# Kernel tuning notes

Hardware: AMD Instinct MI355X
Metric: run time of the kernel (lower is better)

## Reference

```python
import jax, jax.numpy as jnp
import numpy as np

D, H, E, C, B = 1024, 2048, 8, 1024, 8192


def setup_inputs() -> dict:
    key = jax.random.key(0)
    ks = jax.random.split(key, 12)
    s_d = 1.0 / np.sqrt(D)
    s_h = 1.0 / np.sqrt(H)
    return {
        "x": jax.random.normal(ks[0], (B, D), dtype=jnp.float32),
        # gate (Router): Linear(D,D) -> relu -> Linear(D,E) -> softmax
        "gate_w1": jax.random.normal(ks[1], (D, D), dtype=jnp.float32) * s_d,
        "gate_b1": jax.random.normal(ks[2], (D,), dtype=jnp.float32) * s_d,
        "gate_w2": jax.random.normal(ks[3], (D, E), dtype=jnp.float32) * s_d,
        "gate_b2": jax.random.normal(ks[4], (E,), dtype=jnp.float32) * s_d,
        # experts stacked: fc1 [E,D,H], fc2 [E,H,H]
        "W1": jax.random.normal(ks[5], (E, D, H), dtype=jnp.float32) * s_d,
        "b1": jax.random.normal(ks[6], (E, H), dtype=jnp.float32) * s_d,
        "W2": jax.random.normal(ks[7], (E, H, H), dtype=jnp.float32) * s_h,
        "b2": jax.random.normal(ks[8], (E, H), dtype=jnp.float32) * s_h,
        # classifier Linear(H, C)
        "clf_w": jax.random.normal(ks[9], (H, C), dtype=jnp.float32) * s_h,
        "clf_b": jax.random.normal(ks[10], (C,), dtype=jnp.float32) * s_h,
    }


def reference(x, gate_w1, gate_b1, gate_w2, gate_b2, W1, b1, W2, b2, clf_w, clf_b):
    # Router: softmax over experts (dim=1)
    g = jax.nn.relu(x @ gate_w1 + gate_b1)          # [B, D]
    scores = jax.nn.softmax(g @ gate_w2 + gate_b2, axis=1)  # [B, E]

    # All experts, dense (training-mode forward): batched GEMMs over E
    h = jax.nn.relu(jnp.einsum('bd,edh->beh', x, W1) + b1[None])   # [B, E, H]
    expert_outs = jnp.einsum('beh,ehk->bek', h, W2) + b2[None]      # [B, E, H]

    # Shared classifier applied per (token, expert)
    logits = jnp.einsum('beh,hc->bec', expert_outs, clf_w) + clf_b  # [B, E, C]
    return logits, scores
```

## Files before the change

kernel.cpp:

```cpp
#include <hip/hip_runtime.h>
#include <stdint.h>

#define B_DIM 8192
#define D_DIM 1024
#define H_DIM 2048
#define E_DIM 8
#define C_DIM 1024

typedef _Float16 f16x8 __attribute__((ext_vector_type(8)));
typedef float f32x4 __attribute__((ext_vector_type(4)));

__device__ __forceinline__ void store_val(float* p, float v) { *p = v; }
__device__ __forceinline__ void store_val(_Float16* p, float v) { *p = (_Float16)v; }

__device__ __forceinline__ void async_cp16(const void* g, void* l) {
  __builtin_amdgcn_global_load_lds((const __attribute__((address_space(1))) void*)g,
                                   (__attribute__((address_space(3))) void*)l, 16, 0, 0);
}

template <bool RELU, bool BIAS, typename OUT_T>
__global__ void __launch_bounds__(256) gemm_bt(
    const _Float16* __restrict__ A, long aZ,
    const _Float16* __restrict__ Bt, long bZ,
    const float* __restrict__ bias, long biasZ,
    OUT_T* __restrict__ out, long outZ,
    int K, long rs)
{
  __shared__ _Float16 ldsA[128 * 64];
  __shared__ _Float16 ldsB[128 * 64];

  const int z = blockIdx.z;
  A   += (size_t)z * aZ;
  Bt  += (size_t)z * bZ;
  if (BIAS) bias += (size_t)z * biasZ;
  out += (size_t)z * outZ;

  const int tid  = threadIdx.x;
  const int wave = tid >> 6;
  const int lane = tid & 63;
  const int q    = lane >> 4;
  const int l16  = lane & 15;
  const int l8   = lane >> 3;
  const int l7   = lane & 7;

  const int m0   = blockIdx.y * 128;
  const int n0   = blockIdx.x * 128;
  const int wrow = (wave >> 1) * 64;
  const int wcol = (wave & 1) * 64;

  const int swz_st = ((l7 ^ l8) << 3);
  const _Float16* pa[4];
  const _Float16* pb[4];
#pragma unroll
  for (int i = 0; i < 4; ++i) {
    int ci = wave * 4 + i;
    pa[i] = A  + (size_t)(m0 + ci * 8 + l8) * K + swz_st;
    pb[i] = Bt + (size_t)(n0 + ci * 8 + l8) * K + swz_st;
  }

  int a_off[2][4], b_off[2][4];
#pragma unroll
  for (int kk = 0; kk < 2; ++kk) {
#pragma unroll
    for (int r = 0; r < 4; ++r) {
      int sw = ((kk * 4 + q) ^ (l16 & 7)) << 4;
      a_off[kk][r] = (wrow + r * 16 + l16) * 128 + sw;
      b_off[kk][r] = (wcol + r * 16 + l16) * 128 + sw;
    }
  }

  f32x4 acc[4][4];
#pragma unroll
  for (int r = 0; r < 4; ++r)
#pragma unroll
    for (int c = 0; c < 4; ++c)
      acc[r][c] = (f32x4){0.f, 0.f, 0.f, 0.f};

  const char* lAc = (const char*)ldsA;
  const char* lBc = (const char*)ldsB;

  for (int kt = 0; kt < K; kt += 64) {
    __syncthreads();
#pragma unroll
    for (int i = 0; i < 4; ++i) {
      int ci = wave * 4 + i;
      async_cp16(pa[i], ldsA + ci * 512);
      async_cp16(pb[i], ldsB + ci * 512);
      pa[i] += 64;
      pb[i] += 64;
    }
    __syncthreads();
#pragma unroll
    for (int kk = 0; kk < 2; ++kk) {
      f16x8 af[4], bfv[4];
#pragma unroll
      for (int r = 0; r < 4; ++r) af[r]  = *(const f16x8*)(lAc + a_off[kk][r]);
#pragma unroll
      for (int c = 0; c < 4; ++c) bfv[c] = *(const f16x8*)(lBc + b_off[kk][c]);
#pragma unroll
      for (int r = 0; r < 4; ++r)
#pragma unroll
        for (int c = 0; c < 4; ++c)
          acc[r][c] = __builtin_amdgcn_mfma_f32_16x16x32_f16(af[r], bfv[c], acc[r][c], 0, 0, 0);
    }
  }

#pragma unroll
  for (int c = 0; c < 4; ++c) {
    int col = n0 + wcol + c * 16 + l16;
    float bv = BIAS ? bias[col] : 0.f;
#pragma unroll
    for (int r = 0; r < 4; ++r) {
      int row = m0 + wrow + r * 16 + q * 4;
      f32x4 v = acc[r][c];
#pragma unroll
      for (int i = 0; i < 4; ++i) {
        float xv = v[i] + bv;
        if (RELU) xv = fmaxf(xv, 0.f);
        store_val(out + (size_t)(row + i) * rs + col, xv);
      }
    }
  }
}

template <bool RELU, bool BIAS, typename OUT_T>
__global__ void __launch_bounds__(512) gemm256(
    const _Float16* __restrict__ A, long aZ,
    const _Float16* __restrict__ Bt, long bZ,
    const float* __restrict__ bias, long biasZ,
    OUT_T* __restrict__ out, long outZ,
    int K, long rs)
{
  __shared__ _Float16 ldsA[2 * 256 * 64];
  __shared__ _Float16 ldsB[2 * 256 * 64];

  const int z = blockIdx.z;
  A   += (size_t)z * aZ;
  Bt  += (size_t)z * bZ;
  if (BIAS) bias += (size_t)z * biasZ;
  out += (size_t)z * outZ;

  const int nwg = gridDim.x * gridDim.y;
  const int wg  = blockIdx.y * gridDim.x + blockIdx.x;
  const int sw  = (wg & 7) * (nwg >> 3) + (wg >> 3);
  const int bx  = sw % gridDim.x;
  const int by  = sw / gridDim.x;

  const int tid  = threadIdx.x;
  const int wave = tid >> 6;
  const int lane = tid & 63;
  const int q    = lane >> 4;
  const int l16  = lane & 15;
  const int l8   = lane >> 3;
  const int l7   = lane & 7;

  const int m0   = by * 256;
  const int n0   = bx * 256;
  const int wm   = wave >> 2;
  const int wn   = wave & 3;
  const int wrow = wm * 128;
  const int wcol = wn * 64;

  const int swz_st = ((l7 ^ l8) << 3);
  const _Float16* paB = A  + (size_t)(m0 + wave * 16 + l8) * K + swz_st;
  const _Float16* pbB = Bt + (size_t)(n0 + wave * 16 + l8) * K + swz_st;

  int a_base[2], b_base[2];
#pragma unroll
  for (int kk = 0; kk < 2; ++kk) {
    int swr = (((kk * 4 + q) ^ (l16 & 7)) << 4);
    a_base[kk] = (wrow + l16) * 128 + swr;
    b_base[kk] = (wcol + l16) * 128 + swr;
  }

  f32x4 acc[8][4];
#pragma unroll
  for (int r = 0; r < 8; ++r)
#pragma unroll
    for (int c = 0; c < 4; ++c)
      acc[r][c] = (f32x4){0.f, 0.f, 0.f, 0.f};

  const char* lA = (const char*)ldsA;
  const char* lB = (const char*)ldsB;
  const int NT = K >> 6;

#define STAGE_A(buf, h, tt)                                                          \
  {                                                                                  \
    _Pragma("unroll")                                                                \
    for (int i_ = 0; i_ < 2; ++i_)                                                   \
      async_cp16(paB + (size_t)((h) * 128 + i_ * 8) * K + (tt) * 64,                 \
                 (void*)(ldsA + (buf) * 16384 + (h) * 8192 + (wave * 2 + i_) * 512)); \
  }
#define STAGE_B(buf, h, tt)                                                          \
  {                                                                                  \
    _Pragma("unroll")                                                                \
    for (int i_ = 0; i_ < 2; ++i_)                                                   \
      async_cp16(pbB + (size_t)((h) * 128 + i_ * 8) * K + (tt) * 64,                 \
                 (void*)(ldsB + (buf) * 16384 + (h) * 8192 + (wave * 2 + i_) * 512)); \
  }

  STAGE_A(0, 0, 0) STAGE_A(0, 1, 0) STAGE_B(0, 0, 0) STAGE_B(0, 1, 0)
  STAGE_B(1, 0, 1) STAGE_B(1, 1, 1)
  asm volatile("s_waitcnt vmcnt(4)" ::: "memory");
  __builtin_amdgcn_s_barrier();

  for (int t = 0; t < NT; ++t) {
    const int bofs = (t & 1) * 32768;
    f16x8 bf[4][2];
#pragma unroll
    for (int p = 0; p < 4; ++p) {
      f16x8 af[2][2];
#pragma unroll
      for (int rr = 0; rr < 2; ++rr)
#pragma unroll
        for (int kk = 0; kk < 2; ++kk)
          af[rr][kk] = *(const f16x8*)(lA + bofs + a_base[kk] + (2 * p + rr) * 2048);
      if (p == 0) {
#pragma unroll
        for (int c = 0; c < 4; ++c)
#pragma unroll
          for (int kk = 0; kk < 2; ++kk)
            bf[c][kk] = *(const f16x8*)(lB + bofs + b_base[kk] + c * 2048);
      }
      if (p == 0 && t + 1 < NT) STAGE_A((t + 1) & 1, 0, t + 1)
      if (p == 1 && t + 1 < NT) STAGE_A((t + 1) & 1, 1, t + 1)
      if (p == 2 && t + 2 < NT) STAGE_B(t & 1, 0, t + 2)
      if (p == 3 && t + 2 < NT) STAGE_B(t & 1, 1, t + 2)

      __builtin_amdgcn_s_barrier();
      asm volatile("s_waitcnt lgkmcnt(0)" ::: "memory");
      __builtin_amdgcn_sched_barrier(0);
      __builtin_amdgcn_s_setprio(1);
#pragma unroll
      for (int c = 0; c < 4; ++c)
#pragma unroll
        for (int rr = 0; rr < 2; ++rr)
#pragma unroll
          for (int kk = 0; kk < 2; ++kk)
            acc[2 * p + rr][c] = __builtin_amdgcn_mfma_f32_16x16x32_f16(
                af[rr][kk], bf[c][kk], acc[2 * p + rr][c], 0, 0, 0);
      __builtin_amdgcn_s_setprio(0);
      if (p == 3) {
        if (t < NT - 2) asm volatile("s_waitcnt vmcnt(4)" ::: "memory");
        else            asm volatile("s_waitcnt vmcnt(0)" ::: "memory");
      }
      __builtin_amdgcn_s_barrier();
    }
  }
#undef STAGE_A
#undef STAGE_B

#pragma unroll
  for (int c = 0; c < 4; ++c) {
    int col = n0 + wcol + c * 16 + l16;
    float bv = BIAS ? bias[col] : 0.f;
#pragma unroll
    for (int r = 0; r < 8; ++r) {
      int row = m0 + wrow + r * 16 + q * 4;
      f32x4 v = acc[r][c];
#pragma unroll
      for (int i = 0; i < 4; ++i) {
        float xv = v[i] + bv;
        if (RELU) xv = fmaxf(xv, 0.f);
        store_val(out + (size_t)(row + i) * rs + col, xv);
      }
    }
  }
}

__global__ void cast_f32_f16(const float* __restrict__ in, _Float16* __restrict__ out, int n) {
  int i = (blockIdx.x * blockDim.x + threadIdx.x) * 4;
  if (i >= n) return;
  float4 v = *(const float4*)(in + i);
  union { _Float16 h[4]; uint2 u; } r;
  r.h[0] = (_Float16)v.x; r.h[1] = (_Float16)v.y;
  r.h[2] = (_Float16)v.z; r.h[3] = (_Float16)v.w;
  *(uint2*)(out + i) = r.u;
}

__global__ void transpose_cast(const float* __restrict__ in, _Float16* __restrict__ out,
                               int R, int Cn) {
  __shared__ float tile[32][33];
  in  += (size_t)blockIdx.z * R * Cn;
  out += (size_t)blockIdx.z * R * Cn;
  int c0 = blockIdx.x * 32, r0 = blockIdx.y * 32;
  int tx = threadIdx.x, ty = threadIdx.y;
#pragma unroll
  for (int i = ty; i < 32; i += 8)
    tile[i][tx] = in[(size_t)(r0 + i) * Cn + c0 + tx];
  __syncthreads();
#pragma unroll
  for (int i = ty; i < 32; i += 8)
    out[(size_t)(c0 + i) * R + r0 + tx] = (_Float16)tile[tx][i];
}

__global__ void gate2_softmax(const _Float16* __restrict__ g, const float* __restrict__ w2,
                              const float* __restrict__ b2, float* __restrict__ scores) {
  int b = blockIdx.x;
  int t = threadIdx.x;
  int e = t & 7, slice = t >> 3;
  const _Float16* gr = g + (size_t)b * D_DIM;
  float acc = 0.f;
  for (int d = slice; d < D_DIM; d += 32)
    acc += (float)gr[d] * w2[d * 8 + e];
  __shared__ float red[256];
  red[t] = acc;
  __syncthreads();
  for (int s = 16; s > 0; s >>= 1) {
    if (slice < s) red[t] += red[t + s * 8];
    __syncthreads();
  }
  __shared__ float sm[8];
  if (t < 8) sm[t] = red[t] + b2[t];
  __syncthreads();
  if (t == 0) {
    float mx = sm[0];
#pragma unroll
    for (int i = 1; i < 8; ++i) mx = fmaxf(mx, sm[i]);
    float ex[8], s = 0.f;
#pragma unroll
    for (int i = 0; i < 8; ++i) { ex[i] = expf(sm[i] - mx); s += ex[i]; }
    float inv = 1.f / s;
#pragma unroll
    for (int i = 0; i < 8; ++i) scores[(size_t)b * 8 + i] = ex[i] * inv;
  }
}

__global__ void combined_bias(const float* __restrict__ b2, const float* __restrict__ cw,
                              const float* __restrict__ cb, float* __restrict__ bc) {
  int e  = blockIdx.y;
  int cl = threadIdx.x & 63;
  int c  = blockIdx.x * 64 + cl;
  int ks = threadIdx.x >> 6;
  float acc = 0.f;
  for (int k = ks; k < H_DIM; k += 4)
    acc += b2[e * H_DIM + k] * cw[(size_t)k * C_DIM + c];
  __shared__ float red[256];
  red[threadIdx.x] = acc;
  __syncthreads();
  if (ks == 0)
    bc[(size_t)e * C_DIM + c] = red[cl] + red[cl + 64] + red[cl + 128] + red[cl + 192] + cb[c];
}

extern "C" void kernel_launch(void* const* d_in, const int* in_sizes, int n_in,
                              void* d_out, int out_size, void* d_ws, size_t ws_size,
                              hipStream_t stream) {
  const float* x   = (const float*)d_in[0];
  const float* gw1 = (const float*)d_in[1];
  const float* gb1 = (const float*)d_in[2];
  const float* gw2 = (const float*)d_in[3];
  const float* gb2 = (const float*)d_in[4];
  const float* W1  = (const float*)d_in[5];
  const float* b1  = (const float*)d_in[6];
  const float* W2  = (const float*)d_in[7];
  const float* b2  = (const float*)d_in[8];
  const float* cw  = (const float*)d_in[9];
  const float* cb  = (const float*)d_in[10];

  char* ws = (char*)d_ws;
  _Float16* xb     = (_Float16*)(ws);
  _Float16* g      = (_Float16*)(ws + 16777216ull);
  _Float16* gw1t   = (_Float16*)(ws + 33554432ull);
  _Float16* W1t    = (_Float16*)(ws + 35651584ull);
  _Float16* W2c    = (_Float16*)(ws + 69206016ull);
  _Float16* cwt    = (_Float16*)(ws + 136314880ull);
  _Float16* WcombT = (_Float16*)(ws + 140509184ull);
  float*    bc     = (float*)   (ws + 174063616ull);
  _Float16* h_all  = (_Float16*)(ws + 174096384ull);

  float* logits = (float*)d_out;
  float* scores = logits + (size_t)B_DIM * E_DIM * C_DIM;

  cast_f32_f16<<<B_DIM * D_DIM / 4 / 256, 256, 0, stream>>>(x, xb, B_DIM * D_DIM);
  transpose_cast<<<dim3(32, 32, 1), dim3(32, 8), 0, stream>>>(gw1, gw1t, D_DIM, D_DIM);
  transpose_cast<<<dim3(64, 32, 8), dim3(32, 8), 0, stream>>>(W1, W1t, D_DIM, H_DIM);
  cast_f32_f16<<<E_DIM * H_DIM * H_DIM / 4 / 256, 256, 0, stream>>>(W2, W2c, E_DIM * H_DIM * H_DIM);
  transpose_cast<<<dim3(32, 64, 1), dim3(32, 8), 0, stream>>>(cw, cwt, H_DIM, C_DIM);

  gemm_bt<true, true, _Float16><<<dim3(8, 64, 1), 256, 0, stream>>>(
      xb, 0, gw1t, 0, gb1, 0, g, 0, D_DIM, (long)D_DIM);
  gate2_softmax<<<B_DIM, 256, 0, stream>>>(g, gw2, gb2, scores);

  gemm_bt<false, false, _Float16><<<dim3(16, 8, 8), 256, 0, stream>>>(
      cwt, 0, W2c, (long)H_DIM * H_DIM, nullptr, 0,
      WcombT, (long)C_DIM * H_DIM, H_DIM, (long)H_DIM);
  combined_bias<<<dim3(C_DIM / 64, E_DIM), 256, 0, stream>>>(b2, cw, cb, bc);

  gemm256<true, true, _Float16><<<dim3(8, 32, 8), 512, 0, stream>>>(
      xb, 0, W1t, (long)H_DIM * D_DIM, b1, (long)H_DIM,
      h_all, (long)B_DIM * H_DIM, D_DIM, (long)H_DIM);

  gemm256<false, true, float><<<dim3(4, 32, 8), 512, 0, stream>>>(
      h_all, (long)B_DIM * H_DIM, WcombT, (long)C_DIM * H_DIM, bc, (long)C_DIM,
      logits, (long)C_DIM, H_DIM, (long)(E_DIM * C_DIM));
}
```

Baseline: 1.442 ms.

## Template K, restructure gemm256 inner loop, use it for combined-weight GEMM

Makes K a compile-time template parameter and replaces index arithmetic with advancing pointers. The inner loop is reordered to split work by k-half instead of row-pair, keeping fewer fragment registers live. It also drops the mid-phase barrier and waits on LDS reads after the MFMAs rather than before. The classifier-times-W2 combined-weight GEMM moves from the 128-tile gemm_bt to the 256-tile gemm256 kernel. The aim is less register pressure and sync overhead per phase, at the risk of a race on the LDS buffer now that a barrier is gone.

```diff
diff --git a/kernel.cpp b/kernel.cpp
--- a/kernel.cpp
+++ b/kernel.cpp
@@ -123,14 +123,14 @@
   }
 }
 
-template <bool RELU, bool BIAS, typename OUT_T>
+template <bool RELU, bool BIAS, typename OUT_T, int K_CT>
 __global__ void __launch_bounds__(512) gemm256(
     const _Float16* __restrict__ A, long aZ,
     const _Float16* __restrict__ Bt, long bZ,
     const float* __restrict__ bias, long biasZ,
-    OUT_T* __restrict__ out, long outZ,
-    int K, long rs)
+    OUT_T* __restrict__ out, long outZ, long rs)
 {
+  constexpr int NT = K_CT / 64;
   __shared__ _Float16 ldsA[2 * 256 * 64];
   __shared__ _Float16 ldsB[2 * 256 * 64];
 
@@ -162,8 +162,8 @@
   const int wcol = wn * 64;
 
   const int swz_st = ((l7 ^ l8) << 3);
-  const _Float16* paB = A  + (size_t)(m0 + wave * 16 + l8) * K + swz_st;
-  const _Float16* pbB = Bt + (size_t)(n0 + wave * 16 + l8) * K + swz_st;
+  const _Float16* paB = A  + (size_t)(m0 + wave * 16 + l8) * K_CT + swz_st;
+  const _Float16* pbB = Bt + (size_t)(n0 + wave * 16 + l8) * K_CT + swz_st;
 
   int a_base[2], b_base[2];
 #pragma unroll
@@ -182,70 +182,72 @@
 
   const char* lA = (const char*)ldsA;
   const char* lB = (const char*)ldsB;
-  const int NT = K >> 6;
-
-#define STAGE_A(buf, h, tt)                                                          \
-  {                                                                                  \
-    _Pragma("unroll")                                                                \
-    for (int i_ = 0; i_ < 2; ++i_)                                                   \
-      async_cp16(paB + (size_t)((h) * 128 + i_ * 8) * K + (tt) * 64,                 \
-                 (void*)(ldsA + (buf) * 16384 + (h) * 8192 + (wave * 2 + i_) * 512)); \
-  }
-#define STAGE_B(buf, h, tt)                                                          \
-  {                                                                                  \
-    _Pragma("unroll")                                                                \
-    for (int i_ = 0; i_ < 2; ++i_)                                                   \
-      async_cp16(pbB + (size_t)((h) * 128 + i_ * 8) * K + (tt) * 64,                 \
-                 (void*)(ldsB + (buf) * 16384 + (h) * 8192 + (wave * 2 + i_) * 512)); \
-  }
-
-  STAGE_A(0, 0, 0) STAGE_A(0, 1, 0) STAGE_B(0, 0, 0) STAGE_B(0, 1, 0)
-  STAGE_B(1, 0, 1) STAGE_B(1, 1, 1)
+
+#define STAGE_A(bufe, hh, ptr)                                                        \
+  {                                                                                   \
+    _Pragma("unroll")                                                                 \
+    for (int i_ = 0; i_ < 2; ++i_)                                                    \
+      async_cp16((ptr) + (size_t)((hh) * 128 + i_ * 8) * K_CT,                        \
+                 (void*)(ldsA + (bufe) + (hh) * 8192 + (wave * 2 + i_) * 512));       \
+  }
+#define STAGE_B(bufe, hh, ptr)                                                        \
+  {                                                                                   \
+    _Pragma("unroll")                                                                 \
+    for (int i_ = 0; i_ < 2; ++i_)                                                    \
+      async_cp16((ptr) + (size_t)((hh) * 128 + i_ * 8) * K_CT,                        \
+                 (void*)(ldsB + (bufe) + (hh) * 8192 + (wave * 2 + i_) * 512));       \
+  }
+
+  STAGE_A(0, 0, paB) STAGE_A(0, 1, paB)
+  STAGE_B(0, 0, pbB) STAGE_B(0, 1, pbB)
+  STAGE_B(16384, 0, pbB + 64) STAGE_B(16384, 1, pbB + 64)
   asm volatile("s_waitcnt vmcnt(4)" ::: "memory");
   __builtin_amdgcn_s_barrier();
 
+  const _Float16* pa_t = paB + 64;
+  const _Float16* pb_t = pbB + 128;
+
   for (int t = 0; t < NT; ++t) {
-    const int bofs = (t & 1) * 32768;
-    f16x8 bf[4][2];
+    const int bofs  = (t & 1) * 32768;
+    const int nbufe = ((t + 1) & 1) * 16384;
+    const int cbufe = (t & 1) * 16384;
+    f16x8 bf[4];
 #pragma unroll
     for (int p = 0; p < 4; ++p) {
-      f16x8 af[2][2];
-#pragma unroll
-      for (int rr = 0; rr < 2; ++rr)
-#pragma unroll
-        for (int kk = 0; kk < 2; ++kk)
-          af[rr][kk] = *(const f16x8*)(lA + bofs + a_base[kk] + (2 * p + rr) * 2048);
-      if (p == 0) {
+      const int kk = p >> 1, h = p & 1;
+      if (h == 0) {
 #pragma unroll
         for (int c = 0; c < 4; ++c)
-#pragma unroll
-          for (int kk = 0; kk < 2; ++kk)
-            bf[c][kk] = *(const f16x8*)(lB + bofs + b_base[kk] + c * 2048);
+          bf[c] = *(const f16x8*)(lB + bofs + b_base[kk] + c * 2048);
       }
-      if (p == 0 && t + 1 < NT) STAGE_A((t + 1) & 1, 0, t + 1)
-      if (p == 1 && t + 1 < NT) STAGE_A((t + 1) & 1, 1, t + 1)
-      if (p == 2 && t + 2 < NT) STAGE_B(t & 1, 0, t + 2)
-      if (p == 3 && t + 2 < NT) STAGE_B(t & 1, 1, t + 2)
-
-      __builtin_amdgcn_s_barrier();
-      asm volatile("s_waitcnt lgkmcnt(0)" ::: "memory");
-      __builtin_amdgcn_sched_barrier(0);
+      f16x8 af[4];
+#pragma unroll
+      for (int r = 0; r < 4; ++r)
+        af[r] = *(const f16x8*)(lA + bofs + a_base[kk] + (h * 4 + r) * 2048);
+
+      if (p == 0 && t + 1 < NT) STAGE_A(nbufe, 0, pa_t)
+      if (p == 1 && t + 1 < NT) STAGE_A(nbufe, 1, pa_t)
+      if (p == 3 && t + 2 < NT) { STAGE_B(cbufe, 0, pb_t) STAGE_B(cbufe, 1, pb_t) }
+
       __builtin_amdgcn_s_setprio(1);
 #pragma unroll
       for (int c = 0; c < 4; ++c)
 #pragma unroll
-        for (int rr = 0; rr < 2; ++rr)
-#pragma unroll
-          for (int kk = 0; kk < 2; ++kk)
-            acc[2 * p + rr][c] = __builtin_amdgcn_mfma_f32_16x16x32_f16(
-                af[rr][kk], bf[c][kk], acc[2 * p + rr][c], 0, 0, 0);
+        for (int r = 0; r < 4; ++r)
+          acc[h * 4 + r][c] = __builtin_amdgcn_mfma_f32_16x16x32_f16(
+              af[r], bf[c], acc[h * 4 + r][c], 0, 0, 0);
       __builtin_amdgcn_s_setprio(0);
+
       if (p == 3) {
-        if (t < NT - 2) asm volatile("s_waitcnt vmcnt(4)" ::: "memory");
-        else            asm volatile("s_waitcnt vmcnt(0)" ::: "memory");
+        if (t < NT - 2) asm volatile("s_waitcnt vmcnt(4) lgkmcnt(0)" ::: "memory");
+        else            asm volatile("s_waitcnt vmcnt(0) lgkmcnt(0)" ::: "memory");
+      } else {
+        asm volatile("s_waitcnt lgkmcnt(0)" ::: "memory");
       }
       __builtin_amdgcn_s_barrier();
     }
+    pa_t += 64;
+    pb_t += 64;
   }
 #undef STAGE_A
 #undef STAGE_B
@@ -381,16 +383,16 @@
       xb, 0, gw1t, 0, gb1, 0, g, 0, D_DIM, (long)D_DIM);
   gate2_softmax<<<B_DIM, 256, 0, stream>>>(g, gw2, gb2, scores);
 
-  gemm_bt<false, false, _Float16><<<dim3(16, 8, 8), 256, 0, stream>>>(
+  gemm256<false, false, _Float16, H_DIM><<<dim3(8, 4, 8), 512, 0, stream>>>(
       cwt, 0, W2c, (long)H_DIM * H_DIM, nullptr, 0,
-      WcombT, (long)C_DIM * H_DIM, H_DIM, (long)H_DIM);
+      WcombT, (long)C_DIM * H_DIM, (long)H_DIM);
   combined_bias<<<dim3(C_DIM / 64, E_DIM), 256, 0, stream>>>(b2, cw, cb, bc);
 
-  gemm256<true, true, _Float16><<<dim3(8, 32, 8), 512, 0, stream>>>(
+  gemm256<true, true, _Float16, D_DIM><<<dim3(8, 32, 8), 512, 0, stream>>>(
       xb, 0, W1t, (long)H_DIM * D_DIM, b1, (long)H_DIM,
-      h_all, (long)B_DIM * H_DIM, D_DIM, (long)H_DIM);
-
-  gemm256<false, true, float><<<dim3(4, 32, 8), 512, 0, stream>>>(
+      h_all, (long)B_DIM * H_DIM, (long)H_DIM);
+
+  gemm256<false, true, float, H_DIM><<<dim3(4, 32, 8), 512, 0, stream>>>(
       h_all, (long)B_DIM * H_DIM, WcombT, (long)C_DIM * H_DIM, bc, (long)C_DIM,
-      logits, (long)C_DIM, H_DIM, (long)(E_DIM * C_DIM));
-}
+      logits, (long)C_DIM, (long)(E_DIM * C_DIM));
+}
```

Result: faster. 1.406 ms (-2.5%).
